# Performance work log

Measured on AMD Instinct MI355X. Metric: run time of the kernel, lower is better.

The kernel has to match this reference:

```python
import jax, jax.numpy as jnp
import numpy as np

B, S, D, H, DK, DFF = 4, 2048, 512, 8, 64, 2048
MAX_DIST = 2047  # effective_dist = min(MAX_DIST, S-1) = S-1, required by the skew reshape
EPS = 1e-6


def setup_inputs() -> dict:
    key = jax.random.key(0)
    ks = jax.random.split(key, 12)
    w = lambda k, shape: jax.random.normal(k, shape, jnp.float32) * 0.02
    return {
        "x": jax.random.normal(ks[0], (B, S, D), jnp.float32),
        "mask": jnp.tril(jnp.ones((1, 1, S, S), jnp.int32)),  # causal
        "wq": w(ks[1], (D, D)),
        "wk": w(ks[2], (D, D)),
        "wv": w(ks[3], (D, D)),
        "w0": w(ks[4], (D, D)),
        "b0": jnp.zeros((D,), jnp.float32),
        "rel_emb": w(ks[5], (H, MAX_DIST + 1, DK)),
        "ln1_g": jnp.ones((D,), jnp.float32),
        "ln1_b": jnp.zeros((D,), jnp.float32),
        "ln2_g": jnp.ones((D,), jnp.float32),
        "ln2_b": jnp.zeros((D,), jnp.float32),
        "ff_w1": w(ks[6], (D, DFF)),
        "ff_b1": jnp.zeros((DFF,), jnp.float32),
        "ff_w2": w(ks[7], (DFF, D)),
        "ff_b2": jnp.zeros((D,), jnp.float32),
    }


def _layernorm(t, g, b):
    mu = t.mean(-1, keepdims=True)
    var = ((t - mu) ** 2).mean(-1, keepdims=True)
    return (t - mu) * jax.lax.rsqrt(var + EPS) * g + b


def _rel_scores(q, rel_emb):
    # q: [B,H,S,DK]; rel_emb: [H, MAX_DIST+1, DK]
    eff = min(MAX_DIST, S - 1)                      # static
    q_er = jnp.einsum('bhid,hrd->bhir', q, rel_emb[:, :eff + 1])  # [B,H,S,S]
    padded = jnp.pad(q_er, ((0, 0), (0, 0), (0, 0), (1, 0)))      # [B,H,S,S+1]
    # skew trick: reinterpret and drop first row -> [B,H,S,S]
    return padded.reshape(B, H, S + 1, S)[:, :, 1:, :]


def reference(x, mask, wq, wk, wv, w0, b0, rel_emb,
              ln1_g, ln1_b, ln2_g, ln2_b, ff_w1, ff_b1, ff_w2, ff_b2):
    scale = float(np.sqrt(DK))
    # --- self-attention sublayer (pre-norm residual) ---
    h = _layernorm(x, ln1_g, ln1_b)
    q = (h @ wq).reshape(B, S, H, DK).transpose(0, 2, 1, 3)  # [B,H,S,DK]
    k = (h @ wk).reshape(B, S, H, DK).transpose(0, 2, 1, 3)
    v = (h @ wv).reshape(B, S, H, DK).transpose(0, 2, 1, 3)
    content = jnp.einsum('bhid,bhjd->bhij', q, k) / scale     # [B,H,S,S]
    scores = content + _rel_scores(q, rel_emb)
    scores = jnp.where(mask == 0, jnp.float32(-1e9), scores)
    probs = jax.nn.softmax(scores, axis=-1)
    attn = jnp.einsum('bhij,bhjd->bhid', probs, v)            # [B,H,S,DK]
    attn = attn.transpose(0, 2, 1, 3).reshape(B, S, D)
    x = x + (attn @ w0 + b0)
    # --- feed-forward sublayer (pre-norm residual) ---
    h2 = _layernorm(x, ln2_g, ln2_b)
    ff = jax.nn.relu(h2 @ ff_w1 + ff_b1) @ ff_w2 + ff_b2
    return x + ff
```

## Files before the change

### kernel.cpp

```cpp
#include <hip/hip_runtime.h>
#include <hip/hip_bf16.h>

#define SB 2048
#define DB 512
#define HB 8
#define DKB 64
#define DFB 2048
#define BATCH 4
#define BSTR 92

typedef __attribute__((ext_vector_type(8))) short bf16x8;
typedef __attribute__((ext_vector_type(4))) float f32x4;
typedef __attribute__((ext_vector_type(2))) float f32x2;
typedef __attribute__((ext_vector_type(2))) unsigned u32x2;
typedef __attribute__((ext_vector_type(4))) short s16x4;

static __device__ __forceinline__ short f2bf(float x) {
  union { float f; unsigned u; } v; v.f = x;
  unsigned r = (v.u + 0x7fffu + ((v.u >> 16) & 1u)) >> 16;
  return (short)(unsigned short)r;
}

static __device__ __forceinline__ float bflo(unsigned u) {
  union { unsigned x; float f; } v; v.x = u << 16; return v.f;
}
static __device__ __forceinline__ float bfhi(unsigned u) {
  union { unsigned x; float f; } v; v.x = u & 0xffff0000u; return v.f;
}

static __device__ __forceinline__ unsigned pack2bf(float a, float b) {
  return (unsigned)(unsigned short)f2bf(a) | ((unsigned)(unsigned short)f2bf(b) << 16);
}

static __device__ __forceinline__ f32x4 mfma16(bf16x8 a, bf16x8 b, f32x4 c) {
  return __builtin_amdgcn_mfma_f32_16x16x32_bf16(a, b, c, 0, 0, 0);
}

static __device__ __forceinline__ void gload_lds16(const short* g, short* l) {
  __builtin_amdgcn_global_load_lds(
      (const __attribute__((address_space(1))) unsigned*)g,
      (__attribute__((address_space(3))) unsigned*)l, 16, 0, 0);
}

__global__ __launch_bounds__(256) void conv_kernel(const float* __restrict__ src,
                                                   short* __restrict__ dst, int n) {
  int i = blockIdx.x * 256 + threadIdx.x;
  if (i < n) dst[i] = f2bf(src[i]);
}

__global__ __launch_bounds__(256) void tconv_kernel(const float* __restrict__ src,
                                                    short* __restrict__ dst,
                                                    int K, int N, float scale) {
  __shared__ float t[64][65];
  int n0 = blockIdx.x * 64, k0 = blockIdx.y * 64;
  int cn = threadIdx.x & 63, rk = threadIdx.x >> 6;
#pragma unroll
  for (int r = 0; r < 16; ++r)
    t[rk + r * 4][cn] = src[(size_t)(k0 + rk + r * 4) * N + n0 + cn];
  __syncthreads();
#pragma unroll
  for (int r = 0; r < 16; ++r)
    dst[(size_t)(n0 + rk + r * 4) * K + k0 + cn] = f2bf(t[cn][rk + r * 4] * scale);
}

__global__ __launch_bounds__(256) void ln_kernel(const float* __restrict__ in,
                                                 const float* __restrict__ g,
                                                 const float* __restrict__ bb,
                                                 short* __restrict__ out) {
  int w = threadIdx.x >> 6, l = threadIdx.x & 63;
  size_t row = (size_t)blockIdx.x * 4 + w;
  const float* xr = in + row * DB;
  f32x4 v0 = *(const f32x4*)(xr + l * 8);
  f32x4 v1 = *(const f32x4*)(xr + l * 8 + 4);
  float s = (v0[0] + v0[1]) + (v0[2] + v0[3]) + (v1[0] + v1[1]) + (v1[2] + v1[3]);
  float s2 = (v0[0] * v0[0] + v0[1] * v0[1]) + (v0[2] * v0[2] + v0[3] * v0[3]) +
             (v1[0] * v1[0] + v1[1] * v1[1]) + (v1[2] * v1[2] + v1[3] * v1[3]);
#pragma unroll
  for (int off = 1; off < 64; off <<= 1) {
    s += __shfl_xor(s, off, 64);
    s2 += __shfl_xor(s2, off, 64);
  }
  float mean = s * (1.f / DB);
  float var = s2 * (1.f / DB) - mean * mean;
  float rstd = rsqrtf(var + 1e-6f);
  f32x4 g0 = *(const f32x4*)(g + l * 8);
  f32x4 g1 = *(const f32x4*)(g + l * 8 + 4);
  f32x4 b0 = *(const f32x4*)(bb + l * 8);
  f32x4 b1 = *(const f32x4*)(bb + l * 8 + 4);
  bf16x8 ov;
#pragma unroll
  for (int e = 0; e < 4; ++e) ov[e] = f2bf((v0[e] - mean) * rstd * g0[e] + b0[e]);
#pragma unroll
  for (int e = 0; e < 4; ++e) ov[4 + e] = f2bf((v1[e] - mean) * rstd * g1[e] + b1[e]);
  *(bf16x8*)(out + row * DB + l * 8) = ov;
}

template <int KD, int EPI>
__global__ __launch_bounds__(256) void gemm_kernel(
    const short* __restrict__ A, const short* __restrict__ BT,
    const float* __restrict__ bias, const float* __restrict__ resid,
    short* __restrict__ o0, short* __restrict__ o1, short* __restrict__ o2,
    float* __restrict__ of) {
  __shared__ short As[2][4096];
  __shared__ short Bs[2][4096];
  int tid = threadIdx.x;
  int l = tid & 63, w = tid >> 6;
  int wr = w >> 1, wc = w & 1;
  int lr = l & 15, lq = l >> 4;
  int row0 = blockIdx.y * 128;
  int col0 = blockIdx.x * 128;

  f32x4 acc[4][4];
#pragma unroll
  for (int a = 0; a < 4; ++a)
#pragma unroll
    for (int b = 0; b < 4; ++b) acc[a][b] = (f32x4){0.f, 0.f, 0.f, 0.f};

  const short* gA = A + (size_t)(row0 + (tid >> 2)) * KD + (tid & 3) * 8;
  const short* gB = BT + (size_t)(col0 + (tid >> 2)) * KD + (tid & 3) * 8;
  const size_t step64 = (size_t)64 * KD;
  int woff = w * 512;

  auto stage = [&](int buf, int k0) {
    gload_lds16(gA + k0, As[buf] + woff);
    gload_lds16(gA + step64 + k0, As[buf] + woff + 2048);
    gload_lds16(gB + k0, Bs[buf] + woff);
    gload_lds16(gB + step64 + k0, Bs[buf] + woff + 2048);
  };

  stage(0, 0);
  __syncthreads();
  int cur = 0;
  for (int k0 = 0; k0 < KD; k0 += 32) {
    if (k0 + 32 < KD) stage(cur ^ 1, k0 + 32);
    bf16x8 af[4], bfv[4];
#pragma unroll
    for (int a = 0; a < 4; ++a)
      af[a] = *(const bf16x8*)(As[cur] + (wr * 64 + a * 16 + lr) * 32 + lq * 8);
#pragma unroll
    for (int b = 0; b < 4; ++b)
      bfv[b] = *(const bf16x8*)(Bs[cur] + (wc * 64 + b * 16 + lr) * 32 + lq * 8);
#pragma unroll
    for (int a = 0; a < 4; ++a)
#pragma unroll
      for (int b = 0; b < 4; ++b)
        acc[a][b] = mfma16(af[a], bfv[b], acc[a][b]);
    __syncthreads();
    cur ^= 1;
  }

#pragma unroll
  for (int a = 0; a < 4; ++a)
#pragma unroll
    for (int b = 0; b < 4; ++b) {
      size_t colb = (size_t)col0 + wc * 64 + b * 16 + lr;
      if (EPI == 0 && (int)(colb >> 9) == 2) {
        int d = (int)(colb & 63);
        size_t rowb = (size_t)row0 + wr * 64 + a * 16 + lq * 4;
        size_t b_ = rowb >> 11, s_ = rowb & 2047;
        size_t bh = b_ * HB + (int)((colb >> 6) & 7);
        s16x4 pkv;
#pragma unroll
        for (int r = 0; r < 4; ++r) pkv[r] = f2bf(acc[a][b][r]);
        *(s16x4*)(o2 + (bh * DKB + d) * SB + s_) = pkv;
        continue;
      }
#pragma unroll
      for (int r = 0; r < 4; ++r) {
        size_t row = (size_t)row0 + wr * 64 + a * 16 + lq * 4 + r;
        size_t col = colb;
        float val = acc[a][b][r];
        if (EPI == 0) {
          int sect = (int)(col >> 9);
          int hh = (int)((col >> 6) & 7);
          int d = (int)(col & 63);
          size_t b_ = row >> 11, s_ = row & 2047;
          size_t bh = b_ * HB + hh;
          short bv = f2bf(val);
          if (sect == 0) o0[(bh * SB + s_) * DKB + d] = bv;
          else o1[(bh * SB + s_) * DKB + d] = bv;
        } else if (EPI == 1) {
          of[row * DB + col] = resid[row * DB + col] + val + bias[col];
        } else {
          float tv = val + bias[col];
          o0[row * DFB + col] = f2bf(tv > 0.f ? tv : 0.f);
        }
      }
    }
}

template <int KD>
__global__ __launch_bounds__(256) void gemm64_kernel(
    const short* __restrict__ A, const short* __restrict__ BT,
    const float* __restrict__ bias, const float* __restrict__ resid,
    float* __restrict__ of) {
  __shared__ short As[2][4096];
  __shared__ short Bs[2][2048];
  int tid = threadIdx.x;
  int l = tid & 63, w = tid >> 6;
  int lr = l & 15, lq = l >> 4;
  int row0 = blockIdx.y * 128;
  int col0 = blockIdx.x * 64;

  f32x4 acc[2][4];
#pragma unroll
  for (int a = 0; a < 2; ++a)
#pragma unroll
    for (int b = 0; b < 4; ++b) acc[a][b] = (f32x4){0.f, 0.f, 0.f, 0.f};

  const short* gA = A + (size_t)(row0 + (tid >> 2)) * KD + (tid & 3) * 8;
  const short* gB = BT + (size_t)(col0 + (tid >> 2)) * KD + (tid & 3) * 8;
  const size_t step64 = (size_t)64 * KD;
  int woff = w * 512;

  auto stage = [&](int buf, int k0) {
    gload_lds16(gA + k0, As[buf] + woff);
    gload_lds16(gA + step64 + k0, As[buf] + woff + 2048);
    gload_lds16(gB + k0, Bs[buf] + woff);
  };

  stage(0, 0);
  __syncthreads();
  int cur = 0;
  for (int k0 = 0; k0 < KD; k0 += 32) {
    if (k0 + 32 < KD) stage(cur ^ 1, k0 + 32);
    bf16x8 af[2], bfv[4];
#pragma unroll
    for (int a = 0; a < 2; ++a)
      af[a] = *(const bf16x8*)(As[cur] + (w * 32 + a * 16 + lr) * 32 + lq * 8);
#pragma unroll
    for (int b = 0; b < 4; ++b)
      bfv[b] = *(const bf16x8*)(Bs[cur] + (b * 16 + lr) * 32 + lq * 8);
#pragma unroll
    for (int a = 0; a < 2; ++a)
#pragma unroll
      for (int b = 0; b < 4; ++b)
        acc[a][b] = mfma16(af[a], bfv[b], acc[a][b]);
    __syncthreads();
    cur ^= 1;
  }

#pragma unroll
  for (int a = 0; a < 2; ++a)
#pragma unroll
    for (int b = 0; b < 4; ++b)
#pragma unroll
      for (int r = 0; r < 4; ++r) {
        size_t row = (size_t)row0 + w * 32 + a * 16 + lq * 4 + r;
        size_t col = (size_t)col0 + b * 16 + lr;
        of[row * DB + col] = resid[row * DB + col] + acc[a][b][r] + bias[col];
      }
}

static __device__ __forceinline__ void e_phase_lds(const short* Ebuf, int w,
                                                   bf16x8 q0, bf16x8 q1,
                                                   short* bdx, int lr, int lq) {
  bf16x8 ef[10];
#pragma unroll
  for (int nt = 0; nt < 5; ++nt) {
    int re = 48 - 16 * w + nt * 16 + lr;
    const short* eb = Ebuf + re * 64;
    ef[nt * 2] = *(const bf16x8*)(eb + ((lq ^ (re & 7)) << 3));
    ef[nt * 2 + 1] = *(const bf16x8*)(eb + (((lq + 4) ^ (re & 7)) << 3));
  }
  const f32x4 zz = {0.f, 0.f, 0.f, 0.f};
#pragma unroll
  for (int nt = 0; nt < 5; ++nt) {
    f32x4 rr = mfma16(ef[nt * 2 + 1], q1, mfma16(ef[nt * 2], q0, zz));
    u32x2 pk = {pack2bf(rr[0], rr[1]), pack2bf(rr[2], rr[3])};
    *(u32x2*)((char*)bdx + lr * (BSTR * 2) + (nt * 16 + lq * 4) * 2) = pk;
  }
}

static __device__ __forceinline__ void sm_step(const f32x4* sc, const short* bd,
                                               short* pb, f32x4* acc,
                                               float& mrun, float& lsum,
                                               int i0, int j0, int lr, int lq) {
  int bbase = lq * 4 + 15 - lr;
  int o = bbase & 3;
  unsigned shb = (unsigned)(o & 1) * 16;
  bool hi2 = (o >= 2);
  float bv[4][4];
#pragma unroll
  for (int hh = 0; hh < 4; ++hh) {
    int w0 = (hh * 16 + bbase) & ~3;
    const unsigned* p = (const unsigned*)(bd + lr * BSTR + w0);
    unsigned W0 = p[0], W1 = p[1], W2 = p[2], W3 = p[3];
    unsigned X0 = hi2 ? W1 : W0;
    unsigned X1 = hi2 ? W2 : W1;
    unsigned X2 = hi2 ? W3 : W2;
    unsigned out0 = (unsigned)((((unsigned long long)X1 << 32) | X0) >> shb);
    unsigned out1 = (unsigned)((((unsigned long long)X2 << 32) | X1) >> shb);
    bv[hh][0] = bflo(out0);
    bv[hh][1] = bfhi(out0);
    bv[hh][2] = bflo(out1);
    bv[hh][3] = bfhi(out1);
  }
  float s[4][4];
  if (j0 + 63 > i0) {
    int thr = i0 + lr - j0;
#pragma unroll
    for (int hh = 0; hh < 4; ++hh)
#pragma unroll
      for (int r = 0; r < 4; ++r) {
        int n = hh * 16 + lq * 4 + r;
        float v = sc[hh][r] + bv[hh][r];
        s[hh][r] = (n <= thr) ? v : -1e30f;
      }
  } else {
#pragma unroll
    for (int hh = 0; hh < 4; ++hh)
#pragma unroll
      for (int r = 0; r < 4; ++r) s[hh][r] = sc[hh][r] + bv[hh][r];
  }
  float m0 = fmaxf(fmaxf(s[0][0], s[0][1]), fmaxf(s[0][2], s[0][3]));
  float m1 = fmaxf(fmaxf(s[1][0], s[1][1]), fmaxf(s[1][2], s[1][3]));
  float m2 = fmaxf(fmaxf(s[2][0], s[2][1]), fmaxf(s[2][2], s[2][3]));
  float m3 = fmaxf(fmaxf(s[3][0], s[3][1]), fmaxf(s[3][2], s[3][3]));
  float tm = fmaxf(fmaxf(m0, m1), fmaxf(m2, m3));
  if (!__all(tm <= mrun + 8.f)) {
    float tr = fmaxf(tm, __shfl_xor(tm, 16, 64));
    tr = fmaxf(tr, __shfl_xor(tr, 32, 64));
    float mnew = fmaxf(mrun, tr);
    float corr = __expf(mrun - mnew);
    mrun = mnew;
    lsum *= corr;
#pragma unroll
    for (int dt = 0; dt < 4; ++dt) acc[dt] *= corr;
  }
#pragma unroll
  for (int hh = 0; hh < 4; ++hh) {
    float p0 = __expf(s[hh][0] - mrun);
    float p1 = __expf(s[hh][1] - mrun);
    float p2 = __expf(s[hh][2] - mrun);
    float p3 = __expf(s[hh][3] - mrun);
    lsum += (p0 + p1) + (p2 + p3);
    u32x2 pk = {pack2bf(p0, p1), pack2bf(p2, p3)};
    int byteoff = lr * (BSTR * 2) + ((((hh << 1) | (lq >> 1)) ^ (lr & 7)) << 4) + ((lq & 1) << 3);
    *(u32x2*)((char*)pb + byteoff) = pk;
  }
}

static __device__ __forceinline__ void pv_step(const short* pb, const bf16x8* vf,
                                               f32x4* acc, int lr, int lq) {
#pragma unroll
  for (int kc = 0; kc < 2; ++kc) {
    bf16x8 pf = *(const bf16x8*)((const char*)pb + lr * (BSTR * 2) +
                                 ((((kc << 2) | lq) ^ (lr & 7)) << 4));
    __builtin_amdgcn_s_setprio(1);
#pragma unroll
    for (int dt = 0; dt < 4; ++dt)
      acc[dt] = mfma16(vf[kc * 4 + dt], pf, acc[dt]);
    __builtin_amdgcn_s_setprio(0);
  }
}

static __device__ __forceinline__ void attn_out(const f32x4* acc, float lsum,
                                                short* out, int bh, int i0,
                                                int lr, int lq) {
  float lt = lsum + __shfl_xor(lsum, 16, 64);
  lt += __shfl_xor(lt, 32, 64);
  float inv = 1.f / lt;
  int b_ = bh >> 3, hd = bh & 7;
  short* orow = out + ((size_t)(b_ * SB + i0 + lr) * DB + hd * 64);
#pragma unroll
  for (int dt = 0; dt < 4; ++dt) {
    s16x4 pkv;
#pragma unroll
    for (int r = 0; r < 4; ++r) pkv[r] = f2bf(acc[dt][r] * inv);
    *(s16x4*)(orow + dt * 16 + lq * 4) = pkv;
  }
}

__global__ __launch_bounds__(256, 2) void attn_kernel(
    const short* __restrict__ Q, const short* __restrict__ Kb,
    const short* __restrict__ VT, const short* __restrict__ Eb,
    short* __restrict__ out) {
  __shared__ short Ks[4096];
  __shared__ short Vs[4096];
  __shared__ short Elo_s[8192];
  __shared__ short Ehi_s[8192];
  __shared__ short bandP[4][2][16][BSTR];
  int tid = threadIdx.x;
  int l = tid & 63, w = tid >> 6;
  int lr = l & 15, lq = l >> 4;
  int bid = blockIdx.x;
  int s = bid >> 3;
  int bh = (bid & 7) * 4 + (s >> 4);
  int g = s & 15;
  int qb0 = g << 6;
  int qb1 = (31 - g) << 6;
  int i0lo = qb0 + (w << 4);
  int i0hi = qb1 + (w << 4);
  const short* Qh = Q + (size_t)bh * SB * DKB;
  const short* Kh = Kb + (size_t)bh * SB * DKB;
  const short* Vh = VT + (size_t)bh * DKB * SB;
  const short* Eh = Eb + (size_t)(bh & 7) * SB * DKB;

  bf16x8 ql0 = *(const bf16x8*)(Qh + (size_t)(i0lo + lr) * DKB + lq * 8);
  bf16x8 ql1 = *(const bf16x8*)(Qh + (size_t)(i0lo + lr) * DKB + 32 + lq * 8);
  bf16x8 qh0 = *(const bf16x8*)(Qh + (size_t)(i0hi + lr) * DKB + lq * 8);
  bf16x8 qh1 = *(const bf16x8*)(Qh + (size_t)(i0hi + lr) * DKB + 32 + lq * 8);

  int lrow = l >> 3, lch = l & 7;
  int rKV = (w << 4) + lrow;
  int cKV = lch ^ (rKV & 7);
  int rE = (w << 5) + lrow;
  int cE = lch ^ (rE & 7);

  const f32x4 zz = {0.f, 0.f, 0.f, 0.f};
  f32x4 accL[4], accH[4];
#pragma unroll
  for (int dt = 0; dt < 4; ++dt) { accL[dt] = zz; accH[dt] = zz; }
  float mL = -1e30f, lsL = 0.f, mH = -1e30f, lsH = 0.f;
  short* bdL = &bandP[w][0][0][0];
  short* bdH = &bandP[w][1][0][0];

  for (int j0 = 0; j0 < qb1 + 64; j0 += 64) {
    gload_lds16(Kh + (size_t)(j0 + rKV) * DKB + cKV * 8, Ks + (w << 10));
    gload_lds16(Kh + (size_t)(j0 + rKV + 8) * DKB + cKV * 8, Ks + (w << 10) + 512);
    gload_lds16(Vh + (size_t)rKV * SB + j0 + cKV * 8, Vs + (w << 10));
    gload_lds16(Vh + (size_t)(rKV + 8) * SB + j0 + cKV * 8, Vs + (w << 10) + 512);
    int rbHi = SB - 64 - qb1 + j0;
#pragma unroll
    for (int ii = 0; ii < 4; ++ii) {
      int er = rbHi + rE + ii * 8;
      er = er < SB ? er : SB - 1;
      gload_lds16(Eh + (size_t)er * DKB + cE * 8, Ehi_s + (w << 11) + ii * 512);
    }
    if (j0 <= qb0 + 63) {
      int rbLo = SB - 64 - qb0 + j0;
#pragma unroll
      for (int ii = 0; ii < 4; ++ii) {
        int er = rbLo + rE + ii * 8;
        er = er < SB ? er : SB - 1;
        gload_lds16(Eh + (size_t)er * DKB + cE * 8, Elo_s + (w << 11) + ii * 512);
      }
    }
    __syncthreads();
    bool actHi = (j0 <= i0hi + 15);
    bool actLo = (j0 <= i0lo + 15);
    if (actHi) {
      bf16x8 kf[8];
#pragma unroll
      for (int hh = 0; hh < 4; ++hh) {
        int rk = hh * 16 + lr;
        const short* kb = Ks + rk * 64;
        kf[hh * 2] = *(const bf16x8*)(kb + ((lq ^ (rk & 7)) << 3));
        kf[hh * 2 + 1] = *(const bf16x8*)(kb + (((lq + 4) ^ (rk & 7)) << 3));
      }
      f32x4 scH[4], scL[4];
#pragma unroll
      for (int hh = 0; hh < 4; ++hh)
        scH[hh] = mfma16(kf[hh * 2 + 1], qh1, mfma16(kf[hh * 2], qh0, zz));
      if (actLo) {
#pragma unroll
        for (int hh = 0; hh < 4; ++hh)
          scL[hh] = mfma16(kf[hh * 2 + 1], ql1, mfma16(kf[hh * 2], ql0, zz));
      }
      bf16x8 vf[8];
#pragma unroll
      for (int kc = 0; kc < 2; ++kc)
#pragma unroll
        for (int dt = 0; dt < 4; ++dt) {
          int rv = dt * 16 + lr;
          vf[kc * 4 + dt] = *(const bf16x8*)(Vs + rv * 64 +
                                             (((kc * 4 + lq) ^ (rv & 7)) << 3));
        }
      e_phase_lds(Ehi_s, w, qh0, qh1, bdH, lr, lq);
      if (actLo) e_phase_lds(Elo_s, w, ql0, ql1, bdL, lr, lq);
      sm_step(scH, bdH, bdH, accH, mH, lsH, i0hi, j0, lr, lq);
      if (actLo) sm_step(scL, bdL, bdL, accL, mL, lsL, i0lo, j0, lr, lq);
      pv_step(bdH, vf, accH, lr, lq);
      if (actLo) pv_step(bdL, vf, accL, lr, lq);
    }
    __syncthreads();
  }
  attn_out(accH, lsH, out, bh, i0hi, lr, lq);
  attn_out(accL, lsL, out, bh, i0lo, lr, lq);
}

extern "C" void kernel_launch(void* const* d_in, const int* in_sizes, int n_in,
                              void* d_out, int out_size, void* d_ws, size_t ws_size,
                              hipStream_t stream) {
  const float* x    = (const float*)d_in[0];
  const float* wq   = (const float*)d_in[2];
  const float* wk   = (const float*)d_in[3];
  const float* wv   = (const float*)d_in[4];
  const float* w0   = (const float*)d_in[5];
  const float* b0   = (const float*)d_in[6];
  const float* rel  = (const float*)d_in[7];
  const float* ln1g = (const float*)d_in[8];
  const float* ln1b = (const float*)d_in[9];
  const float* ln2g = (const float*)d_in[10];
  const float* ln2b = (const float*)d_in[11];
  const float* fw1  = (const float*)d_in[12];
  const float* fb1  = (const float*)d_in[13];
  const float* fw2  = (const float*)d_in[14];
  const float* fb2  = (const float*)d_in[15];
  float* outp = (float*)d_out;

  char* ws = (char*)d_ws;
  size_t off = 0;
  auto alloc = [&](size_t bytes) {
    char* p = ws + off;
    off += (bytes + 255) & ~(size_t)255;
    return p;
  };
  short* wqkvT = (short*)alloc((size_t)1536 * 512 * 2);
  short* w0T   = (short*)alloc((size_t)512 * 512 * 2);
  short* fw1T  = (short*)alloc((size_t)2048 * 512 * 2);
  short* fw2T  = (short*)alloc((size_t)512 * 2048 * 2);
  short* relb  = (short*)alloc((size_t)8 * 2048 * 64 * 2);
  short* hbuf  = (short*)alloc((size_t)8192 * 512 * 2);
  short* Qb    = (short*)alloc((size_t)8192 * 512 * 2);
  short* Kbf   = (short*)alloc((size_t)8192 * 512 * 2);
  short* VTb   = (short*)alloc((size_t)8192 * 512 * 2);
  short* attnb = (short*)alloc((size_t)8192 * 512 * 2);
  float* x2    = (float*)alloc((size_t)8192 * 512 * 4);
  short* ff1 = hbuf;
  short* h2  = attnb;

  dim3 blk(256);
  conv_kernel<<<(8 * 2048 * 64 + 255) / 256, blk, 0, stream>>>(rel, relb, 8 * 2048 * 64);
  tconv_kernel<<<dim3(8, 8), blk, 0, stream>>>(wq, wqkvT, 512, 512, 1.f);
  tconv_kernel<<<dim3(8, 8), blk, 0, stream>>>(wk, wqkvT + 512 * 512, 512, 512, 0.125f);
  tconv_kernel<<<dim3(8, 8), blk, 0, stream>>>(wv, wqkvT + 1024 * 512, 512, 512, 1.f);
  tconv_kernel<<<dim3(8, 8), blk, 0, stream>>>(w0, w0T, 512, 512, 1.f);
  tconv_kernel<<<dim3(32, 8), blk, 0, stream>>>(fw1, fw1T, 512, 2048, 1.f);
  tconv_kernel<<<dim3(8, 32), blk, 0, stream>>>(fw2, fw2T, 2048, 512, 1.f);

  ln_kernel<<<2048, blk, 0, stream>>>(x, ln1g, ln1b, hbuf);
  gemm_kernel<512, 0><<<dim3(12, 64), blk, 0, stream>>>(hbuf, wqkvT, nullptr, nullptr,
                                                        Qb, Kbf, VTb, nullptr);
  attn_kernel<<<512, blk, 0, stream>>>(Qb, Kbf, VTb, relb, attnb);
  gemm64_kernel<512><<<dim3(8, 64), blk, 0, stream>>>(attnb, w0T, b0, x, x2);
  ln_kernel<<<2048, blk, 0, stream>>>(x2, ln2g, ln2b, h2);
  gemm_kernel<512, 2><<<dim3(16, 64), blk, 0, stream>>>(h2, fw1T, fb1, nullptr,
                                                        ff1, nullptr, nullptr, nullptr);
  gemm64_kernel<2048><<<dim3(8, 64), blk, 0, stream>>>(ff1, fw2T, fb2, x2, outp);
}
```

Baseline: 235.3 us.

## Reuse overlapping rel-emb rows via LDS ring buffer; merge attention weight transposes

The attention kernel now keeps the relative-embedding tile in a 128-row circular LDS buffer. On each 64-column step after the first, only the 64 newly needed rows are fetched from global memory instead of reloading all 128, which cuts global-to-LDS traffic for E. The always-true actHi guard is removed. Separately, the four 512x512 weight transpose/convert launches are merged into one 3D-grid launch. The w0 result is written directly after wqkvT and relies on w0T being laid out contiguously after it.

```diff
diff --git a/kernel.cpp b/kernel.cpp
--- a/kernel.cpp
+++ b/kernel.cpp
@@ -61,6 +61,26 @@
 #pragma unroll
   for (int r = 0; r < 16; ++r)
     dst[(size_t)(n0 + rk + r * 4) * K + k0 + cn] = f2bf(t[cn][rk + r * 4] * scale);
+}
+
+__global__ __launch_bounds__(256) void tconv4_kernel(
+    const float* __restrict__ s0, const float* __restrict__ s1,
+    const float* __restrict__ s2, const float* __restrict__ s3,
+    short* __restrict__ dst) {
+  __shared__ float t[64][65];
+  int z = blockIdx.z;
+  const float* src = z == 0 ? s0 : (z == 1 ? s1 : (z == 2 ? s2 : s3));
+  float scale = (z == 1) ? 0.125f : 1.f;
+  short* d = dst + (size_t)z * 512 * 512;
+  int n0 = blockIdx.x * 64, k0 = blockIdx.y * 64;
+  int cn = threadIdx.x & 63, rk = threadIdx.x >> 6;
+#pragma unroll
+  for (int r = 0; r < 16; ++r)
+    t[rk + r * 4][cn] = src[(size_t)(k0 + rk + r * 4) * 512 + n0 + cn];
+  __syncthreads();
+#pragma unroll
+  for (int r = 0; r < 16; ++r)
+    d[(size_t)(n0 + rk + r * 4) * 512 + k0 + cn] = f2bf(t[cn][rk + r * 4] * scale);
 }
 
 __global__ __launch_bounds__(256) void ln_kernel(const float* __restrict__ in,
@@ -252,16 +272,17 @@
       }
 }
 
-static __device__ __forceinline__ void e_phase_lds(const short* Ebuf, int w,
+static __device__ __forceinline__ void e_phase_lds(const short* Ebuf, int w, int ph,
                                                    bf16x8 q0, bf16x8 q1,
                                                    short* bdx, int lr, int lq) {
   bf16x8 ef[10];
 #pragma unroll
   for (int nt = 0; nt < 5; ++nt) {
     int re = 48 - 16 * w + nt * 16 + lr;
-    const short* eb = Ebuf + re * 64;
-    ef[nt * 2] = *(const bf16x8*)(eb + ((lq ^ (re & 7)) << 3));
-    ef[nt * 2 + 1] = *(const bf16x8*)(eb + (((lq + 4) ^ (re & 7)) << 3));
+    int sr = (re + ph) & 127;
+    const short* eb = Ebuf + sr * 64;
+    ef[nt * 2] = *(const bf16x8*)(eb + ((lq ^ (sr & 7)) << 3));
+    ef[nt * 2 + 1] = *(const bf16x8*)(eb + (((lq + 4) ^ (sr & 7)) << 3));
   }
   const f32x4 zz = {0.f, 0.f, 0.f, 0.f};
 #pragma unroll
@@ -405,8 +426,7 @@
   int lrow = l >> 3, lch = l & 7;
   int rKV = (w << 4) + lrow;
   int cKV = lch ^ (rKV & 7);
-  int rE = (w << 5) + lrow;
-  int cE = lch ^ (rE & 7);
+  int cE = lch ^ lrow;
 
   const f32x4 zz = {0.f, 0.f, 0.f, 0.f};
   f32x4 accL[4], accH[4];
@@ -422,25 +442,52 @@
     gload_lds16(Vh + (size_t)rKV * SB + j0 + cKV * 8, Vs + (w << 10));
     gload_lds16(Vh + (size_t)(rKV + 8) * SB + j0 + cKV * 8, Vs + (w << 10) + 512);
     int rbHi = SB - 64 - qb1 + j0;
-#pragma unroll
-    for (int ii = 0; ii < 4; ++ii) {
-      int er = rbHi + rE + ii * 8;
-      er = er < SB ? er : SB - 1;
-      gload_lds16(Eh + (size_t)er * DKB + cE * 8, Ehi_s + (w << 11) + ii * 512);
+    int phHi = rbHi & 64;
+    if (j0 == 0) {
+#pragma unroll
+      for (int ii = 0; ii < 4; ++ii) {
+        int rr = (w << 5) + lrow + ii * 8;
+        int er = rbHi + rr;
+        er = er < SB ? er : SB - 1;
+        int slot0 = ((w << 5) + ii * 8 + phHi) & 127;
+        gload_lds16(Eh + (size_t)er * DKB + cE * 8, Ehi_s + (slot0 << 6));
+      }
+    } else {
+#pragma unroll
+      for (int ii = 0; ii < 2; ++ii) {
+        int rr = (w << 4) + lrow + ii * 8;
+        int er = rbHi + 64 + rr;
+        er = er < SB ? er : SB - 1;
+        int slot0 = ((w << 4) + ii * 8 + (phHi ^ 64)) & 127;
+        gload_lds16(Eh + (size_t)er * DKB + cE * 8, Ehi_s + (slot0 << 6));
+      }
     }
+    int rbLo = SB - 64 - qb0 + j0;
+    int phLo = rbLo & 64;
     if (j0 <= qb0 + 63) {
-      int rbLo = SB - 64 - qb0 + j0;
-#pragma unroll
-      for (int ii = 0; ii < 4; ++ii) {
-        int er = rbLo + rE + ii * 8;
-        er = er < SB ? er : SB - 1;
-        gload_lds16(Eh + (size_t)er * DKB + cE * 8, Elo_s + (w << 11) + ii * 512);
+      if (j0 == 0) {
+#pragma unroll
+        for (int ii = 0; ii < 4; ++ii) {
+          int rr = (w << 5) + lrow + ii * 8;
+          int er = rbLo + rr;
+          er = er < SB ? er : SB - 1;
+          int slot0 = ((w << 5) + ii * 8 + phLo) & 127;
+          gload_lds16(Eh + (size_t)er * DKB + cE * 8, Elo_s + (slot0 << 6));
+        }
+      } else {
+#pragma unroll
+        for (int ii = 0; ii < 2; ++ii) {
+          int rr = (w << 4) + lrow + ii * 8;
+          int er = rbLo + 64 + rr;
+          er = er < SB ? er : SB - 1;
+          int slot0 = ((w << 4) + ii * 8 + (phLo ^ 64)) & 127;
+          gload_lds16(Eh + (size_t)er * DKB + cE * 8, Elo_s + (slot0 << 6));
+        }
       }
     }
     __syncthreads();
-    bool actHi = (j0 <= i0hi + 15);
     bool actLo = (j0 <= i0lo + 15);
-    if (actHi) {
+    {
       bf16x8 kf[8];
 #pragma unroll
       for (int hh = 0; hh < 4; ++hh) {
@@ -467,8 +514,8 @@
           vf[kc * 4 + dt] = *(const bf16x8*)(Vs + rv * 64 +
                                              (((kc * 4 + lq) ^ (rv & 7)) << 3));
         }
-      e_phase_lds(Ehi_s, w, qh0, qh1, bdH, lr, lq);
-      if (actLo) e_phase_lds(Elo_s, w, ql0, ql1, bdL, lr, lq);
+      e_phase_lds(Ehi_s, w, phHi, qh0, qh1, bdH, lr, lq);
+      if (actLo) e_phase_lds(Elo_s, w, phLo, ql0, ql1, bdL, lr, lq);
       sm_step(scH, bdH, bdH, accH, mH, lsH, i0hi, j0, lr, lq);
       if (actLo) sm_step(scL, bdL, bdL, accL, mL, lsL, i0lo, j0, lr, lq);
       pv_step(bdH, vf, accH, lr, lq);
@@ -520,13 +567,11 @@
   float* x2    = (float*)alloc((size_t)8192 * 512 * 4);
   short* ff1 = hbuf;
   short* h2  = attnb;
+  (void)w0T;
 
   dim3 blk(256);
   conv_kernel<<<(8 * 2048 * 64 + 255) / 256, blk, 0, stream>>>(rel, relb, 8 * 2048 * 64);
-  tconv_kernel<<<dim3(8, 8), blk, 0, stream>>>(wq, wqkvT, 512, 512, 1.f);
-  tconv_kernel<<<dim3(8, 8), blk, 0, stream>>>(wk, wqkvT + 512 * 512, 512, 512, 0.125f);
-  tconv_kernel<<<dim3(8, 8), blk, 0, stream>>>(wv, wqkvT + 1024 * 512, 512, 512, 1.f);
-  tconv_kernel<<<dim3(8, 8), blk, 0, stream>>>(w0, w0T, 512, 512, 1.f);
+  tconv4_kernel<<<dim3(8, 8, 4), blk, 0, stream>>>(wq, wk, wv, w0, wqkvT);
   tconv_kernel<<<dim3(32, 8), blk, 0, stream>>>(fw1, fw1T, 512, 2048, 1.f);
   tconv_kernel<<<dim3(8, 32), blk, 0, stream>>>(fw2, fw2T, 2048, 512, 1.f);
 
@@ -534,7 +579,8 @@
   gemm_kernel<512, 0><<<dim3(12, 64), blk, 0, stream>>>(hbuf, wqkvT, nullptr, nullptr,
                                                         Qb, Kbf, VTb, nullptr);
   attn_kernel<<<512, blk, 0, stream>>>(Qb, Kbf, VTb, relb, attnb);
-  gemm64_kernel<512><<<dim3(8, 64), blk, 0, stream>>>(attnb, w0T, b0, x, x2);
+  gemm64_kernel<512><<<dim3(8, 64), blk, 0, stream>>>(attnb, wqkvT + (size_t)3 * 512 * 512,
+                                                      b0, x, x2);
   ln_kernel<<<2048, blk, 0, stream>>>(x2, ln2g, ln2b, h2);
   gemm_kernel<512, 2><<<dim3(16, 64), blk, 0, stream>>>(h2, fw1T, fb1, nullptr,
                                                         ff1, nullptr, nullptr, nullptr);
```

New measurement: 226.8 us. 1.04x faster.
